# Optimization experiments

Hardware: AMD Instinct MI355X
Metric: run time of the kernel (lower is better)

## Reference

```python
import jax, jax.numpy as jnp
import numpy as np

B, S, D = 4, 2048, 1024
H, DK, DV = 16, 64, 64


def setup_inputs() -> dict:
    key = jax.random.key(0)
    ks = jax.random.split(key, 12)
    sd = 0.02
    return {
        "input_query": jax.random.normal(ks[0], (B, S, D), jnp.float32),
        "input_key": jax.random.normal(ks[1], (B, S, D), jnp.float32),
        "input_value": jax.random.normal(ks[2], (B, S, D), jnp.float32),
        "Wq": jax.random.normal(ks[3], (H, D, DK), jnp.float32) * sd,
        "bq": jax.random.normal(ks[4], (H, DK), jnp.float32) * sd,
        "Wk": jax.random.normal(ks[5], (H, D, DK), jnp.float32) * sd,
        "bk": jax.random.normal(ks[6], (H, DK), jnp.float32) * sd,
        "Wv": jax.random.normal(ks[7], (H, D, DV), jnp.float32) * sd,
        "bv": jax.random.normal(ks[8], (H, DV), jnp.float32) * sd,
        "Wo": jax.random.normal(ks[9], (H * DV, D), jnp.float32) * sd,
        "bo": jax.random.normal(ks[10], (D,), jnp.float32) * sd,
    }


def reference(input_query, input_key, input_value, Wq, bq, Wk, bk, Wv, bv, Wo, bo):
    # per-head projections, batched over all heads at once
    q = jnp.einsum("bsd,hdk->bhsk", input_query, Wq) + bq[None, :, None, :]
    k = jnp.einsum("bsd,hdk->bhsk", input_key, Wk) + bk[None, :, None, :]
    v = jnp.einsum("bsd,hdv->bhsv", input_value, Wv) + bv[None, :, None, :]
    # NOTE: original code computes self.dk = sqrt(d_k) but never divides by it,
    # so scores are UNSCALED QK^T (faithful to the source).
    score = jnp.einsum("bhqk,bhsk->bhqs", q, k)  # [B,H,S,S]
    score = jax.nn.softmax(score, axis=-1)
    z = jnp.einsum("bhqs,bhsv->bhqv", score, v)  # [B,H,S,DV]
    # concat heads along feature dim (dim=2 in torch) -> [B,S,H*DV]
    z = jnp.transpose(z, (0, 2, 1, 3)).reshape(z.shape[0], z.shape[2], -1)
    return z @ Wo + bo
```

## Files before the change

kernel.cpp:

```cpp
#include <hip/hip_runtime.h>


using short8  = __attribute__((ext_vector_type(8))) short;
using short4_t= __attribute__((ext_vector_type(4))) short;
using floatx4 = __attribute__((ext_vector_type(4))) float;

#define MFMA32(a, b, c) __builtin_amdgcn_mfma_f32_16x16x32_bf16((a), (b), (c), 0, 0, 0)
#define MFMA16(a, b, c) __builtin_amdgcn_mfma_f32_16x16x16bf16_1k((a), (b), (c), 0, 0, 0)

__device__ __forceinline__ void async16(const unsigned short* g, unsigned short* lds_base) {
  __builtin_amdgcn_global_load_lds(
      (const __attribute__((address_space(1))) unsigned int*)g,
      (__attribute__((address_space(3))) unsigned int*)lds_base, 16, 0, 0);
}

__device__ __forceinline__ float bf2f(unsigned short u) {
  union { unsigned int i; float f; } v; v.i = ((unsigned int)u) << 16; return v.f;
}
__device__ __forceinline__ unsigned short f2bf(float f) {
  union { float f; unsigned int i; } v; v.f = f;
  unsigned int r = v.i + 0x7FFFu + ((v.i >> 16) & 1u);
  return (unsigned short)(r >> 16);
}
__device__ __forceinline__ unsigned int fbits(float f) {
  union { float f; unsigned int i; } v; v.f = f; return v.i;
}
__device__ __forceinline__ unsigned short ld_bf(const void* p, size_t idx, int isbf16) {
  return isbf16 ? ((const unsigned short*)p)[idx] : f2bf(((const float*)p)[idx]);
}
__device__ __forceinline__ float ld_f(const void* p, size_t idx, int isbf16) {
  return isbf16 ? bf2f(((const unsigned short*)p)[idx]) : ((const float*)p)[idx];
}

__global__ void detect_dtype(const unsigned int* __restrict__ X,
                             unsigned int* __restrict__ flag) {
  __shared__ int red[256];
  int cnt = 0;
  for (int i = threadIdx.x; i < 4096; i += 256) {
    unsigned int e = (X[i] >> 7) & 0xFFu;
    cnt += (e >= 96u && e <= 160u) ? 1 : 0;
  }
  red[threadIdx.x] = cnt;
  __syncthreads();
  for (int s = 128; s > 0; s >>= 1) {
    if (threadIdx.x < (unsigned)s) red[threadIdx.x] += red[threadIdx.x + s];
    __syncthreads();
  }
  if (threadIdx.x == 0) *flag = (red[0] >= 2560) ? 1u : 0u;
}

__global__ __launch_bounds__(256) void prep(
    const void* __restrict__ Xq, const void* __restrict__ Xk,
    const void* __restrict__ Xv,
    const void* __restrict__ Wq, const void* __restrict__ Wk,
    const void* __restrict__ Wv, const void* __restrict__ Wo,
    unsigned short* __restrict__ Xqc, unsigned short* __restrict__ Xkc,
    unsigned short* __restrict__ Xvc,
    unsigned short* __restrict__ WT,
    unsigned short* __restrict__ WoT,
    const unsigned int* __restrict__ flagp)
{
  const int isbf16 = (int)*flagp;
  const int bid = blockIdx.x, tid = threadIdx.x;

  if (bid < 12288) {
    const int z = bid >> 12;
    const int i = ((bid & 4095) << 8) + tid;
    const void* X = (z == 0) ? Xq : (z == 1) ? Xk : Xv;
    unsigned short* Y = (z == 0) ? Xqc : (z == 1) ? Xkc : Xvc;
    if (isbf16) {
      ((uint4*)Y)[i] = ((const uint4*)X)[i];
    } else {
      const float* f = (const float*)X + (size_t)i * 8;
      union { unsigned short u[8]; uint4 v; } t;
#pragma unroll
      for (int j = 0; j < 8; ++j) t.u[j] = f2bf(f[j]);
      ((uint4*)Y)[i] = t.v;
    }
    return;
  }

  __shared__ unsigned short tile[32][33];
  const int tx = tid & 31, ty = tid >> 5;
  const int t = bid - 12288;
  if (t < 3072) {
    const int x = t & 1, y = (t >> 1) & 31, zz = t >> 6;
    const int w = zz >> 4, hh = zz & 15;
    const void* in = (w == 0) ? Wq : (w == 1) ? Wk : Wv;
    const size_t boff = (size_t)hh * 1024 * 64;
    unsigned short* op = WT + ((size_t)w << 20) + boff;
    const int r0 = y * 32, c0 = x * 32;
#pragma unroll
    for (int i = 0; i < 4; ++i) {
      int r = ty + i * 8;
      tile[r][tx] = ld_bf(in, boff + (size_t)(r0 + r) * 64 + (c0 + tx), isbf16);
    }
    __syncthreads();
#pragma unroll
    for (int i = 0; i < 4; ++i) {
      int c = ty + i * 8;
      op[(size_t)(c0 + c) * 1024 + (r0 + tx)] = tile[tx][c];
    }
  } else {
    const int t2 = t - 3072;
    const int x = t2 & 31, y = t2 >> 5;
    const int r0 = y * 32, c0 = x * 32;
#pragma unroll
    for (int i = 0; i < 4; ++i) {
      int r = ty + i * 8;
      tile[r][tx] = ld_bf(Wo, (size_t)(r0 + r) * 1024 + (c0 + tx), isbf16);
    }
    __syncthreads();
#pragma unroll
    for (int i = 0; i < 4; ++i) {
      int c = ty + i * 8;
      WoT[(size_t)(c0 + c) * 1024 + (r0 + tx)] = tile[tx][c];
    }
  }
}

#define GEMM_MAIN_LOOP(Aq, Btq, Kdim)                                          \
  floatx4 acc[4][4];                                                           \
  _Pragma("unroll") for (int i = 0; i < 4; ++i)                                \
      _Pragma("unroll") for (int j = 0; j < 4; ++j)                            \
          acc[i][j] = (floatx4){0.f, 0.f, 0.f, 0.f};                           \
  const int lrow = lane >> 3, cg = lane & 7;                                   \
  const int scol = ((cg ^ lrow) * 8);                                          \
  const int sw = ln15 & 7;                                                     \
  for (int k0 = 0; k0 < (Kdim); k0 += 64) {                                    \
    __syncthreads();                                                           \
    _Pragma("unroll") for (int r = 0; r < 4; ++r) {                            \
      const int chunk = r * 4 + wave;                                          \
      const int row = chunk * 8 + lrow;                                        \
      async16(&(Aq)[(size_t)(m0 + row) * (Kdim) + k0 + scol],                  \
              &a_lds[(size_t)chunk * 512]);                                    \
      async16(&(Btq)[(size_t)(n0 + row) * (Kdim) + k0 + scol],                 \
              &b_lds[(size_t)chunk * 512]);                                    \
    }                                                                          \
    __syncthreads();                                                           \
    _Pragma("unroll") for (int kk = 0; kk < 2; ++kk) {                         \
      short8 af[4];                                                            \
      _Pragma("unroll") for (int i = 0; i < 4; ++i)                            \
          af[i] = *(const short8*)&a_lds[(wm + i * 16 + ln15) * 64 +           \
                                         (((kk * 4 + quad) ^ sw) * 8)];        \
      _Pragma("unroll") for (int j = 0; j < 4; ++j) {                          \
        short8 bf = *(const short8*)&b_lds[(wn + j * 16 + ln15) * 64 +         \
                                           (((kk * 4 + quad) ^ sw) * 8)];      \
        _Pragma("unroll") for (int i = 0; i < 4; ++i)                          \
            acc[i][j] = MFMA32(af[i], bf, acc[i][j]);                          \
      }                                                                        \
    }                                                                          \
  }

__global__ __launch_bounds__(256) void gemm_qkv(
    const unsigned short* __restrict__ A0, const unsigned short* __restrict__ A1,
    const unsigned short* __restrict__ A2,
    const unsigned short* __restrict__ BT,
    const void* __restrict__ b0, const void* __restrict__ b1,
    const void* __restrict__ b2,
    unsigned short* __restrict__ Qp, unsigned short* __restrict__ Kp,
    unsigned short* __restrict__ Vt,
    const unsigned int* __restrict__ flagp)
{
  const int isbf16 = (int)*flagp;
  const int z = blockIdx.z;
  const unsigned short* A  = (z == 0) ? A0 : (z == 1) ? A1 : A2;
  const unsigned short* Bt = BT + ((size_t)z << 20);
  const void* bias = (z == 0) ? b0 : (z == 1) ? b1 : b2;
  const int m0 = blockIdx.x * 128, n0 = blockIdx.y * 128;
  const int tid = threadIdx.x, wave = tid >> 6, lane = tid & 63;
  const int ln15 = lane & 15, quad = lane >> 4;
  const int wm = (wave >> 1) * 64, wn = (wave & 1) * 64;
  __shared__ alignas(16) unsigned short a_lds[128 * 64];
  __shared__ alignas(16) unsigned short b_lds[128 * 64];

  GEMM_MAIN_LOOP(A, Bt, 1024)

  if (z < 2) {
    unsigned short* C = z ? Kp : Qp;
#pragma unroll
    for (int j = 0; j < 4; ++j) {
      const int col = n0 + wn + j * 16 + ln15;
      const float bv = ld_f(bias, col, isbf16);
#pragma unroll
      for (int i = 0; i < 4; ++i) {
        const int row = m0 + wm + i * 16 + quad * 4;
#pragma unroll
        for (int r = 0; r < 4; ++r)
          C[(size_t)(row + r) * 1024 + col] = f2bf(acc[i][j][r] + bv);
      }
    }
  } else {
    __syncthreads();
#pragma unroll
    for (int j = 0; j < 4; ++j) {
      const int nl = wn + j * 16 + ln15;
      const float bv = ld_f(bias, n0 + nl, isbf16);
      unsigned short* dst = (nl < 64) ? &a_lds[(size_t)nl * 128]
                                      : &b_lds[(size_t)(nl - 64) * 128];
#pragma unroll
      for (int i = 0; i < 4; ++i) {
        const int ml = wm + i * 16 + quad * 4;
#pragma unroll
        for (int r = 0; r < 4; ++r) dst[ml + r] = f2bf(acc[i][j][r] + bv);
      }
    }
    __syncthreads();
    const int nl = tid >> 1, half = tid & 1;
    const unsigned short* src = (nl < 64) ? &a_lds[(size_t)nl * 128 + half * 64]
                                          : &b_lds[(size_t)(nl - 64) * 128 + half * 64];
    const int bb = m0 >> 11, s0 = m0 & 2047;
    unsigned short* dst = Vt + (size_t)bb * 2048 * 1024 +
                          (size_t)(n0 + nl) * 2048 + s0 + half * 64;
#pragma unroll
    for (int c = 0; c < 8; ++c) *(uint4*)&dst[c * 8] = *(const uint4*)&src[c * 8];
  }
}

__global__ __launch_bounds__(256) void gemm_out(
    const unsigned short* __restrict__ A,
    const unsigned short* __restrict__ Bt,
    const void* __restrict__ bias,
    void* __restrict__ C,
    const unsigned int* __restrict__ flagp)
{
  const int isbf16 = (int)*flagp;
  const int m0 = blockIdx.x * 128, n0 = blockIdx.y * 128;
  const int tid = threadIdx.x, wave = tid >> 6, lane = tid & 63;
  const int ln15 = lane & 15, quad = lane >> 4;
  const int wm = (wave >> 1) * 64, wn = (wave & 1) * 64;
  __shared__ alignas(16) unsigned short a_lds[128 * 64];
  __shared__ alignas(16) unsigned short b_lds[128 * 64];

  GEMM_MAIN_LOOP(A, Bt, 1024)

#pragma unroll
  for (int j = 0; j < 4; ++j) {
    const int col = n0 + wn + j * 16 + ln15;
    const float bv = ld_f(bias, col, isbf16);
#pragma unroll
    for (int i = 0; i < 4; ++i) {
      const int row = m0 + wm + i * 16 + quad * 4;
#pragma unroll
      for (int r = 0; r < 4; ++r) {
        const float val = acc[i][j][r] + bv;
        if (!isbf16) ((float*)C)[(size_t)(row + r) * 1024 + col] = val;
        else ((unsigned short*)C)[(size_t)(row + r) * 1024 + col] = f2bf(val);
      }
    }
  }
}

__global__ __launch_bounds__(256, 2) void attn(
    const unsigned short* __restrict__ Q,
    const unsigned short* __restrict__ K,
    const unsigned short* __restrict__ Vt,
    unsigned short* __restrict__ Z)
{
  const int h = blockIdx.x, b = blockIdx.y, qt0 = blockIdx.z * 256;
  const int tid = threadIdx.x, wave = tid >> 6, lane = tid & 63;
  const int ln15 = lane & 15, quad = lane >> 4;

  __shared__ alignas(16) char smem[55296];
  unsigned short* q_lds = (unsigned short*)smem;
  unsigned short* k_lds = (unsigned short*)(smem + 36864);
  unsigned short* v_lds = (unsigned short*)(smem + 46080);

  const unsigned short* Qb = Q + ((size_t)(b * 2048 + qt0)) * 1024 + h * 64;
  const unsigned short* Kb = K + ((size_t)(b * 2048)) * 1024 + h * 64;
  const unsigned short* Vh = Vt + (size_t)b * 2048 * 1024 + (size_t)h * 64 * 2048;

  const int sr = tid >> 2, sc = (tid & 3) * 16;
#pragma unroll
  for (int i = 0; i < 4; ++i) {
    const int r = sr + i * 64;
    *(uint4*)&q_lds[r * 72 + sc]     = *(const uint4*)&Qb[(size_t)r * 1024 + sc];
    *(uint4*)&q_lds[r * 72 + sc + 8] = *(const uint4*)&Qb[(size_t)r * 1024 + sc + 8];
  }
  __syncthreads();
  short8 qf[4][2];
#pragma unroll
  for (int g = 0; g < 4; ++g) {
    const int row = (g * 4 + wave) * 16 + ln15;
    qf[g][0] = *(const short8*)&q_lds[row * 72 + quad * 8];
    qf[g][1] = *(const short8*)&q_lds[row * 72 + 32 + quad * 8];
  }

  floatx4 o_acc[4][4];
#pragma unroll
  for (int g = 0; g < 4; ++g)
#pragma unroll
    for (int vb = 0; vb < 4; ++vb) o_acc[g][vb] = (floatx4){0.f, 0.f, 0.f, 0.f};
  float l_part[4] = {0.f, 0.f, 0.f, 0.f};

  for (int j0 = 0; j0 < 2048; j0 += 64) {
    __syncthreads();
    *(uint4*)&k_lds[sr * 72 + sc]     = *(const uint4*)&Kb[(size_t)(j0 + sr) * 1024 + sc];
    *(uint4*)&k_lds[sr * 72 + sc + 8] = *(const uint4*)&Kb[(size_t)(j0 + sr) * 1024 + sc + 8];
    *(uint4*)&v_lds[sr * 72 + sc]     = *(const uint4*)&Vh[(size_t)sr * 2048 + j0 + sc];
    *(uint4*)&v_lds[sr * 72 + sc + 8] = *(const uint4*)&Vh[(size_t)sr * 2048 + j0 + sc + 8];
    __syncthreads();

    short8 kf[4][2];
    short4_t vf[4][4];
#pragma unroll
    for (int nb = 0; nb < 4; ++nb) {
      kf[nb][0] = *(const short8*)&k_lds[(nb * 16 + ln15) * 72 + quad * 8];
      kf[nb][1] = *(const short8*)&k_lds[(nb * 16 + ln15) * 72 + 32 + quad * 8];
    }
#pragma unroll
    for (int vb = 0; vb < 4; ++vb)
#pragma unroll
      for (int nb = 0; nb < 4; ++nb)
        vf[vb][nb] = *(const short4_t*)&v_lds[(vb * 16 + ln15) * 72 + nb * 16 + quad * 4];

#pragma unroll
    for (int g = 0; g < 4; ++g) {
      short4_t pb[4];
#pragma unroll
      for (int nb = 0; nb < 4; ++nb) {
        floatx4 st = (floatx4){0.f, 0.f, 0.f, 0.f};
        st = MFMA32(kf[nb][0], qf[g][0], st);
        st = MFMA32(kf[nb][1], qf[g][1], st);
        const float p0 = __expf(st[0]), p1 = __expf(st[1]);
        const float p2 = __expf(st[2]), p3 = __expf(st[3]);
        l_part[g] += (p0 + p1) + (p2 + p3);
        union { unsigned int u[2]; short4_t s; } pk;
        pk.u[0] = __builtin_amdgcn_perm(fbits(p1), fbits(p0), 0x07060302u);
        pk.u[1] = __builtin_amdgcn_perm(fbits(p3), fbits(p2), 0x07060302u);
        pb[nb] = pk.s;
      }
#pragma unroll
      for (int vb = 0; vb < 4; ++vb)
#pragma unroll
        for (int nb = 0; nb < 4; ++nb)
          o_acc[g][vb] = MFMA16(vf[vb][nb], pb[nb], o_acc[g][vb]);
    }
  }

  __syncthreads();
  float* ot = (float*)smem;
  const int q = tid >> 2, vg = (tid & 3) * 16;
#pragma unroll
  for (int g = 0; g < 4; ++g) {
    float l = l_part[g];
    l += __shfl_xor(l, 16);
    l += __shfl_xor(l, 32);
    const float rl = 1.0f / l;
#pragma unroll
    for (int vb = 0; vb < 4; ++vb)
#pragma unroll
      for (int r = 0; r < 4; ++r)
        ot[(wave * 16 + ln15) * 66 + vb * 16 + quad * 4 + r] = o_acc[g][vb][r] * rl;
    __syncthreads();
    union { unsigned short u[16]; uint4 v[2]; } t;
#pragma unroll
    for (int i = 0; i < 16; ++i) t.u[i] = f2bf(ot[q * 66 + vg + i]);
    unsigned short* dst = Z + ((size_t)(b * 2048 + qt0 + g * 64 + q)) * 1024 + h * 64 + vg;
    *(uint4*)&dst[0] = t.v[0];
    *(uint4*)&dst[8] = t.v[1];
    __syncthreads();
  }
}

extern "C" void kernel_launch(void* const* d_in, const int* in_sizes, int n_in,
                              void* d_out, int out_size, void* d_ws, size_t ws_size,
                              hipStream_t stream) {
  const void* Xq = d_in[0];
  const void* Xk = d_in[1];
  const void* Xv = d_in[2];
  const void* Wq = d_in[3];
  const void* bq = d_in[4];
  const void* Wk = d_in[5];
  const void* bk = d_in[6];
  const void* Wv = d_in[7];
  const void* bv = d_in[8];
  const void* Wo = d_in[9];
  const void* bo = d_in[10];

  unsigned int*   flag = (unsigned int*)d_ws;
  unsigned short* base = (unsigned short*)d_ws + 128;
  unsigned short* WqT = base;
  unsigned short* WoT = WqT + (3u << 20);
  unsigned short* buf0 = WoT + (1u << 20);
  unsigned short* buf1 = buf0 + (8u << 20);
  unsigned short* buf2 = buf1 + (8u << 20);
  unsigned short* buf3 = buf2 + (8u << 20);
  unsigned short* buf4 = buf3 + (8u << 20);
  unsigned short* buf5 = buf4 + (8u << 20);
  unsigned short *Xqc = buf0, *Xkc = buf1, *Xvc = buf2;
  unsigned short *Qp = buf3, *Kp = buf4, *VtR = buf5;
  unsigned short *Zp = buf2;

  detect_dtype<<<1, 256, 0, stream>>>((const unsigned int*)Xq, flag);

  prep<<<16384, 256, 0, stream>>>(Xq, Xk, Xv, Wq, Wk, Wv, Wo,
                                  Xqc, Xkc, Xvc, WqT, WoT, flag);

  gemm_qkv<<<dim3(64, 8, 3), 256, 0, stream>>>(Xqc, Xkc, Xvc, WqT, bq, bk, bv,
                                               Qp, Kp, VtR, flag);

  attn<<<dim3(16, 4, 8), 256, 0, stream>>>(Qp, Kp, VtR, Zp);

  gemm_out<<<dim3(64, 8), 256, 0, stream>>>(Zp, WoT, bo, d_out, flag);
}
```

Measured before the change: 350.8 us.

## Shrink attention LDS and register footprint, fold log2e into Q for exp2

```diff
diff --git a/kernel.cpp b/kernel.cpp
--- a/kernel.cpp
+++ b/kernel.cpp
@@ -178,6 +178,7 @@
 
   if (z < 2) {
     unsigned short* C = z ? Kp : Qp;
+    const float scale = z ? 1.0f : 1.4426950408889634f;
 #pragma unroll
     for (int j = 0; j < 4; ++j) {
       const int col = n0 + wn + j * 16 + ln15;
@@ -187,7 +188,7 @@
         const int row = m0 + wm + i * 16 + quad * 4;
 #pragma unroll
         for (int r = 0; r < 4; ++r)
-          C[(size_t)(row + r) * 1024 + col] = f2bf(acc[i][j][r] + bv);
+          C[(size_t)(row + r) * 1024 + col] = f2bf((acc[i][j][r] + bv) * scale);
       }
     }
   } else {
@@ -251,7 +252,7 @@
   }
 }
 
-__global__ __launch_bounds__(256, 2) void attn(
+__global__ __launch_bounds__(256, 3) void attn(
     const unsigned short* __restrict__ Q,
     const unsigned short* __restrict__ K,
     const unsigned short* __restrict__ Vt,
@@ -261,29 +262,20 @@
   const int tid = threadIdx.x, wave = tid >> 6, lane = tid & 63;
   const int ln15 = lane & 15, quad = lane >> 4;
 
-  __shared__ alignas(16) char smem[55296];
-  unsigned short* q_lds = (unsigned short*)smem;
-  unsigned short* k_lds = (unsigned short*)(smem + 36864);
-  unsigned short* v_lds = (unsigned short*)(smem + 46080);
+  __shared__ alignas(16) char smem[18432];
+  unsigned short* k_lds = (unsigned short*)smem;
+  unsigned short* v_lds = (unsigned short*)(smem + 9216);
 
   const unsigned short* Qb = Q + ((size_t)(b * 2048 + qt0)) * 1024 + h * 64;
   const unsigned short* Kb = K + ((size_t)(b * 2048)) * 1024 + h * 64;
   const unsigned short* Vh = Vt + (size_t)b * 2048 * 1024 + (size_t)h * 64 * 2048;
 
-  const int sr = tid >> 2, sc = (tid & 3) * 16;
-#pragma unroll
-  for (int i = 0; i < 4; ++i) {
-    const int r = sr + i * 64;
-    *(uint4*)&q_lds[r * 72 + sc]     = *(const uint4*)&Qb[(size_t)r * 1024 + sc];
-    *(uint4*)&q_lds[r * 72 + sc + 8] = *(const uint4*)&Qb[(size_t)r * 1024 + sc + 8];
-  }
-  __syncthreads();
   short8 qf[4][2];
 #pragma unroll
   for (int g = 0; g < 4; ++g) {
     const int row = (g * 4 + wave) * 16 + ln15;
-    qf[g][0] = *(const short8*)&q_lds[row * 72 + quad * 8];
-    qf[g][1] = *(const short8*)&q_lds[row * 72 + 32 + quad * 8];
+    qf[g][0] = *(const short8*)&Qb[(size_t)row * 1024 + quad * 8];
+    qf[g][1] = *(const short8*)&Qb[(size_t)row * 1024 + 32 + quad * 8];
   }
 
   floatx4 o_acc[4][4];
@@ -292,6 +284,8 @@
 #pragma unroll
     for (int vb = 0; vb < 4; ++vb) o_acc[g][vb] = (floatx4){0.f, 0.f, 0.f, 0.f};
   float l_part[4] = {0.f, 0.f, 0.f, 0.f};
+
+  const int sr = tid >> 2, sc = (tid & 3) * 16;
 
   for (int j0 = 0; j0 < 2048; j0 += 64) {
     __syncthreads();
@@ -301,40 +295,30 @@
     *(uint4*)&v_lds[sr * 72 + sc + 8] = *(const uint4*)&Vh[(size_t)sr * 2048 + j0 + sc + 8];
     __syncthreads();
 
-    short8 kf[4][2];
-    short4_t vf[4][4];
 #pragma unroll
     for (int nb = 0; nb < 4; ++nb) {
-      kf[nb][0] = *(const short8*)&k_lds[(nb * 16 + ln15) * 72 + quad * 8];
-      kf[nb][1] = *(const short8*)&k_lds[(nb * 16 + ln15) * 72 + 32 + quad * 8];
-    }
-#pragma unroll
-    for (int vb = 0; vb < 4; ++vb)
-#pragma unroll
-      for (int nb = 0; nb < 4; ++nb)
-        vf[vb][nb] = *(const short4_t*)&v_lds[(vb * 16 + ln15) * 72 + nb * 16 + quad * 4];
-
-#pragma unroll
-    for (int g = 0; g < 4; ++g) {
-      short4_t pb[4];
-#pragma unroll
-      for (int nb = 0; nb < 4; ++nb) {
+      const short8 kf0 = *(const short8*)&k_lds[(nb * 16 + ln15) * 72 + quad * 8];
+      const short8 kf1 = *(const short8*)&k_lds[(nb * 16 + ln15) * 72 + 32 + quad * 8];
+      short4_t vf[4];
+#pragma unroll
+      for (int vb = 0; vb < 4; ++vb)
+        vf[vb] = *(const short4_t*)&v_lds[(vb * 16 + ln15) * 72 + nb * 16 + quad * 4];
+
+#pragma unroll
+      for (int g = 0; g < 4; ++g) {
         floatx4 st = (floatx4){0.f, 0.f, 0.f, 0.f};
-        st = MFMA32(kf[nb][0], qf[g][0], st);
-        st = MFMA32(kf[nb][1], qf[g][1], st);
-        const float p0 = __expf(st[0]), p1 = __expf(st[1]);
-        const float p2 = __expf(st[2]), p3 = __expf(st[3]);
+        st = MFMA32(kf0, qf[g][0], st);
+        st = MFMA32(kf1, qf[g][1], st);
+        const float p0 = exp2f(st[0]), p1 = exp2f(st[1]);
+        const float p2 = exp2f(st[2]), p3 = exp2f(st[3]);
         l_part[g] += (p0 + p1) + (p2 + p3);
         union { unsigned int u[2]; short4_t s; } pk;
         pk.u[0] = __builtin_amdgcn_perm(fbits(p1), fbits(p0), 0x07060302u);
         pk.u[1] = __builtin_amdgcn_perm(fbits(p3), fbits(p2), 0x07060302u);
-        pb[nb] = pk.s;
+#pragma unroll
+        for (int vb = 0; vb < 4; ++vb)
+          o_acc[g][vb] = MFMA16(vf[vb], pk.s, o_acc[g][vb]);
       }
-#pragma unroll
-      for (int vb = 0; vb < 4; ++vb)
-#pragma unroll
-        for (int nb = 0; nb < 4; ++nb)
-          o_acc[g][vb] = MFMA16(vf[vb][nb], pb[nb], o_acc[g][vb]);
     }
   }
 
```

Result: slower. 650.1 us (+85.3%).
